# Kernel tuning notes

Measured on AMD Instinct MI355X. Metric: run time of the kernel, lower is better.

Reference implementation:

```python
import jax, jax.numpy as jnp
from jax import lax
import numpy as np

K = 1024      # kernel_size
S = 256       # stride
CUT = 513     # kernel_size//2 + 1
TC = 2 * CUT  # transform_channels = 1026
CH = 8        # combine_hidden
B = 32
TIME = 262144


def setup_inputs() -> dict:
    key = jax.random.key(0)
    ks = jax.random.split(key, 12)
    x = jax.random.normal(ks[0], (B, 1, TIME), dtype=jnp.float32)
    conv1_w = jax.random.normal(ks[1], (TC, 1, K), dtype=jnp.float32) * 0.02
    in_gamma = 1.0 + 0.1 * jax.random.normal(ks[2], (TC,), dtype=jnp.float32)
    comb1_w = jax.random.normal(ks[3], (CH, 2), dtype=jnp.float32) * 0.5
    comb1_b = jax.random.normal(ks[4], (CH,), dtype=jnp.float32) * 0.1
    comb2_w = jax.random.normal(ks[5], (1, CH), dtype=jnp.float32) * 0.5
    comb2_b = jax.random.normal(ks[6], (1,), dtype=jnp.float32) * 0.1
    lin_w = jax.random.normal(ks[7], (CUT, CUT), dtype=jnp.float32) * 0.04
    lin_b = jax.random.normal(ks[8], (CUT,), dtype=jnp.float32) * 0.02
    fc_gamma = 1.0 + 0.1 * jax.random.normal(ks[9], (CUT,), dtype=jnp.float32)
    convT_w = jax.random.normal(ks[10], (TC, 2, K), dtype=jnp.float32) * 0.02  # torch ConvTranspose1d (Cin, Cout, K)
    return {"x": x, "conv1_w": conv1_w, "in_gamma": in_gamma,
            "comb1_w": comb1_w, "comb1_b": comb1_b,
            "comb2_w": comb2_w, "comb2_b": comb2_b,
            "lin_w": lin_w, "lin_b": lin_b, "fc_gamma": fc_gamma,
            "convT_w": convT_w}


def reference(x, conv1_w, in_gamma, comb1_w, comb1_b, comb2_w, comb2_b,
              lin_w, lin_b, fc_gamma, convT_w):
    time = x.shape[2]
    # conv1: Conv1d(1, TC, K, stride=S, padding=K), no bias
    t = lax.conv_general_dilated(x, conv1_w, window_strides=(S,),
                                 padding=[(K, K)],
                                 dimension_numbers=("NCH", "OIH", "NCH"))
    # ConvScaler1d (per-channel scale) + tanh activation
    t = jnp.tanh(t * in_gamma[None, :, None])  # (B, TC, F)
    real_x, imag_x = t[:, :CUT, :], t[:, CUT:, :]
    spec = jnp.stack([real_x, imag_x], axis=1)  # (B, 2, CUT, F)
    # combine1/combine2: 1x1 Conv2d + relu
    h = jax.nn.relu(jnp.einsum("bcxf,oc->boxf", spec, comb1_w)
                    + comb1_b[None, :, None, None])
    h = jax.nn.relu(jnp.einsum("bcxf,oc->boxf", h, comb2_w)
                    + comb2_b[None, :, None, None])[:, 0]  # (B, CUT, F)
    # FC over frequency axis per (batch, frame)
    hh = h.transpose(0, 2, 1)  # (B, F, CUT)
    hh = (hh @ lin_w.T + lin_b) * fc_gamma  # BitwiseLinear + Scaler
    mask = (jnp.tanh(hh) + 1.0) * 0.5       # output_transform -> [0,1]
    mask = mask.transpose(0, 2, 1)          # (B, CUT, F)
    mask = jnp.concatenate([mask, mask], axis=1)  # (B, TC, F)
    t = t * mask
    # conv1_transpose: ConvTranspose1d(TC, 2, K, stride=S), no bias
    wt = jnp.flip(convT_w.transpose(1, 0, 2), axis=2)  # (2, TC, K) flipped
    y = lax.conv_general_dilated(t, wt, window_strides=(1,),
                                 padding=[(K - 1, K - 1)],
                                 lhs_dilation=(S,),
                                 dimension_numbers=("NCH", "OIH", "NCH"))
    y = y[:, :, K:time + K]  # (B, 2, time)
    return jax.nn.softmax(y, axis=1)
```

## Files before the change

### kernel.cpp

```cpp
#include <hip/hip_runtime.h>
#include <cstddef>
#include <cstdint>

#define TIME_N 262144
#define BATCH  32
#define KW     1024
#define ST     256
#define CUTN   513
#define TCN    1026
#define FN     1029
#define FPAD   1152
#define CPAD   1152
#define XLEN   (FPAD * ST + KW)
#define XBLK   (XLEN / 256)

#define MROWS  (BATCH * FN)
#define MP     33024
#define KPH    544
#define NPH    640
#define TBP    1040
#define FLATB  (FN * TBP)
#define KPC    4160

#define PB_XPAD  (XBLK * BATCH)
#define PB_WBF   (PB_XPAD + CPAD)
#define PB_WLIN  (PB_WBF + NPH)
#define PB_TOTAL (PB_WLIN + KPC)

typedef __bf16 bf16x8 __attribute__((ext_vector_type(8)));
typedef float floatx4 __attribute__((ext_vector_type(4)));

__device__ __forceinline__ unsigned short f2bf(float f) {
    union { float f; unsigned u; } v; v.f = f;
    unsigned r = (v.u + 0x7fffu + ((v.u >> 16) & 1u)) >> 16;
    return (unsigned short)r;
}
__device__ __forceinline__ float bf2f(unsigned short s) {
    union { unsigned u; float f; } v; v.u = ((unsigned)s) << 16;
    return v.f;
}
__device__ __forceinline__ int permch(int n) {
    return (n & 1) ? (CUTN + (n >> 1)) : (n >> 1);
}

__device__ __forceinline__ void load_lds16(const void* g, void* l) {
    __builtin_amdgcn_global_load_lds(
        (const __attribute__((address_space(1))) void*)g,
        (__attribute__((address_space(3))) void*)l, 16, 0, 0);
}

__global__ __launch_bounds__(256) void k_prep(
    const float* __restrict__ x, const float* __restrict__ c1w,
    const float* __restrict__ lw, const float* __restrict__ wct,
    unsigned short* __restrict__ xb, unsigned short* __restrict__ wbf,
    unsigned short* __restrict__ wlb, unsigned short* __restrict__ wdb)
{
    const int bid = blockIdx.x;
    if (bid < PB_XPAD) {
        const int b = bid / XBLK;
        const int p = (bid - b * XBLK) * 256 + threadIdx.x;
        const int g = p - KW;
        float v = (g >= 0 && g < TIME_N) ? x[(size_t)b * TIME_N + g] : 0.0f;
        xb[(size_t)b * XLEN + p] = f2bf(v);
    } else if (bid < PB_WBF) {
        const int n = bid - PB_XPAD;
        const int ch = (n < TCN) ? permch(n) : 0;
        for (int k = threadIdx.x; k < KW; k += 256) {
            float v = (n < TCN) ? c1w[(size_t)ch * KW + k] : 0.0f;
            wbf[(size_t)n * KW + k] = f2bf(v);
        }
    } else if (bid < PB_WLIN) {
        const int n = bid - PB_WBF;
        for (int k = threadIdx.x; k < KPH; k += 256) {
            float v = (n < CUTN && k < CUTN) ? lw[(size_t)n * CUTN + k] : 0.0f;
            wlb[(size_t)n * KPH + k] = f2bf(v);
        }
    } else {
        const int k = bid - PB_WLIN;
        const int r = threadIdx.x;
        const int j = k / TBP;
        const int n = k - j * TBP;
        float v = 0.0f;
        if (n < TCN) {
            const int ch = permch(n);
            const int widx = (3 - j) * 256 + r;
            v = wct[(size_t)(2 * ch) * KW + widx] -
                wct[(size_t)(2 * ch + 1) * KW + widx];
        }
        wdb[(size_t)r * KPC + k] = f2bf(v);
    }
}

__global__ __launch_bounds__(256) void k_conv1m(
    const unsigned short* __restrict__ xb, const unsigned short* __restrict__ wb,
    const float* __restrict__ gamma,
    const float* __restrict__ c1w, const float* __restrict__ c1b,
    const float* __restrict__ c2w, const float* __restrict__ c2b,
    unsigned short* __restrict__ tb2, unsigned short* __restrict__ h)
{
    extern __shared__ __align__(16) char lds[];

    const int b = blockIdx.x, fb = blockIdx.y, cb = blockIdx.z;
    const int f0 = fb * 128, c0 = cb * 128;
    const int tid = threadIdx.x;

    const unsigned short* xrow = xb + (size_t)b * XLEN;
    const unsigned short* ga[4];
    const unsigned short* gb[4];
    int qa[4];
#pragma unroll
    for (int i = 0; i < 4; ++i) {
        const int c = i * 256 + tid;
        const int row = c >> 3;
        const int colb = (c & 7) * 16;
        const int es = (colb ^ ((row & 7) << 4)) >> 1;
        qa[i] = c * 16;
        ga[i] = xrow + (size_t)(f0 + row) * ST + es;
        gb[i] = wb + (size_t)(c0 + row) * KW + es;
    }

    const int wave = tid >> 6, lane = tid & 63;
    const int lm = lane & 15, lq = lane >> 4;
    const int mw = (wave & 1) * 64, nw = (wave >> 1) * 64;
    const int swz = (lm & 7) << 4;
    int abo[2], bbo[2];
#pragma unroll
    for (int ks = 0; ks < 2; ++ks) {
        abo[ks] = (mw + lm) * 128 + ((ks * 64 + lq * 16) ^ swz);
        bbo[ks] = 16384 + (nw + lm) * 128 + ((ks * 64 + lq * 16) ^ swz);
    }

    floatx4 acc[4][4];
#pragma unroll
    for (int i = 0; i < 4; ++i)
#pragma unroll
        for (int j = 0; j < 4; ++j) acc[i][j] = (floatx4)0.0f;

#pragma unroll
    for (int i = 0; i < 4; ++i) {
        load_lds16(ga[i], lds + qa[i]);
        load_lds16(gb[i], lds + 16384 + qa[i]);
        ga[i] += 64; gb[i] += 64;
    }
    __syncthreads();

    for (int t = 0; t < KW / 64; ++t) {
        char* cur = lds + (t & 1) * 32768;
        char* nxt = lds + ((t + 1) & 1) * 32768;

        if (t + 1 < KW / 64) {
#pragma unroll
            for (int i = 0; i < 4; ++i) {
                load_lds16(ga[i], nxt + qa[i]);
                load_lds16(gb[i], nxt + 16384 + qa[i]);
                ga[i] += 64; gb[i] += 64;
            }
        }

        bf16x8 afr[4][2], bfr[4][2];
#pragma unroll
        for (int mt = 0; mt < 4; ++mt)
#pragma unroll
            for (int ks = 0; ks < 2; ++ks)
                afr[mt][ks] = *(const bf16x8*)(cur + abo[ks] + mt * 2048);
#pragma unroll
        for (int nt = 0; nt < 4; ++nt)
#pragma unroll
            for (int ks = 0; ks < 2; ++ks)
                bfr[nt][ks] = *(const bf16x8*)(cur + bbo[ks] + nt * 2048);
#pragma unroll
        for (int mt = 0; mt < 4; ++mt)
#pragma unroll
            for (int nt = 0; nt < 4; ++nt)
#pragma unroll
                for (int ks = 0; ks < 2; ++ks)
                    acc[mt][nt] = __builtin_amdgcn_mfma_f32_16x16x32_bf16(
                        afr[mt][ks], bfr[nt][ks], acc[mt][nt], 0, 0, 0);
        __syncthreads();
    }

    float w1[16], b1[8], w2[8];
#pragma unroll
    for (int o = 0; o < 8; ++o) {
        w1[2 * o]     = c1w[2 * o];
        w1[2 * o + 1] = c1w[2 * o + 1];
        b1[o] = c1b[o];
        w2[o] = c2w[o];
    }
    const float b2v = c2b[0];

    unsigned short* tbb = tb2 + (size_t)b * FLATB;
    const bool evenlane = ((lane & 1) == 0);
#pragma unroll
    for (int nt = 0; nt < 4; ++nt) {
        const int n = c0 + nw + nt * 16 + lm;
        const bool valid_c = (n < TCN);
        const float gv = valid_c ? gamma[permch(n)] : 0.0f;
        const int nbase = n & ~1;
        const int ybase = n >> 1;
        const bool store_c = (nbase < TBP);
#pragma unroll
        for (int mt = 0; mt < 4; ++mt) {
#pragma unroll
            for (int rp = 0; rp < 2; ++rp) {
                const int ra = rp * 2;
                const int fa = f0 + mw + mt * 16 + lq * 4 + ra;
                const float ua = acc[mt][nt][ra] * gv;
                const float ub = acc[mt][nt][ra + 1] * gv;
                const float ta  = 2.0f / (1.0f + __expf(-2.0f * ua)) - 1.0f;
                const float tbv = 2.0f / (1.0f + __expf(-2.0f * ub)) - 1.0f;
                const float sa = __shfl_xor(ta, 1);
                const float sb = __shfl_xor(tbv, 1);
                const int  fme = evenlane ? fa : (fa + 1);
                const float re = evenlane ? ta : sb;
                const float im = evenlane ? sa : tbv;
                if (fme < FN) {
                    if (store_c) {
                        const unsigned pr = (unsigned)f2bf(re) |
                                            ((unsigned)f2bf(im) << 16);
                        *(unsigned*)&tbb[(size_t)fme * TBP + nbase] = pr;
                    }
                    if (valid_c) {
                        float a2 = b2v;
#pragma unroll
                        for (int o = 0; o < 8; ++o) {
                            const float a1 = fmaxf(
                                re * w1[2 * o] + im * w1[2 * o + 1] + b1[o], 0.0f);
                            a2 += a1 * w2[o];
                        }
                        h[((size_t)b * FN + fme) * KPH + ybase] =
                            f2bf(fmaxf(a2, 0.0f));
                    }
                }
            }
        }
    }
}

__global__ __launch_bounds__(256) void k_maskm(
    const unsigned short* __restrict__ h, const unsigned short* __restrict__ wlb,
    const float* __restrict__ linb, const float* __restrict__ fcg,
    unsigned* __restrict__ tbu)
{
    __shared__ __align__(16) unsigned short As[128 * 32];
    __shared__ __align__(16) unsigned short Bs[128 * 32];

    const int m0 = blockIdx.x * 128, n0 = blockIdx.y * 128;
    const int tid = threadIdx.x;

    const int s0 = tid, s1 = tid + 256;
    const int ar0 = s0 >> 2, aq0 = s0 & 3;
    const int ar1 = s1 >> 2, aq1 = s1 & 3;
    const unsigned short* ga0 = h + (size_t)(m0 + ar0) * KPH + aq0 * 8;
    const unsigned short* ga1 = h + (size_t)(m0 + ar1) * KPH + aq1 * 8;
    const unsigned short* gb0 = wlb + (size_t)(n0 + ar0) * KPH + aq0 * 8;
    const unsigned short* gb1 = wlb + (size_t)(n0 + ar1) * KPH + aq1 * 8;
    unsigned short* la0 = &As[s0 * 8];
    unsigned short* la1 = &As[s1 * 8];
    unsigned short* lb0 = &Bs[s0 * 8];
    unsigned short* lb1 = &Bs[s1 * 8];

    const int wave = tid >> 6, lane = tid & 63;
    const int lm = lane & 15, lq = lane >> 4;
    const int mw = (wave & 1) * 64, nw = (wave >> 1) * 64;
    const unsigned short* Ap = &As[(mw + lm) * 32 + lq * 8];
    const unsigned short* Bp = &Bs[(nw + lm) * 32 + lq * 8];

    floatx4 acc[4][4];
#pragma unroll
    for (int i = 0; i < 4; ++i)
#pragma unroll
        for (int j = 0; j < 4; ++j) acc[i][j] = (floatx4)0.0f;

    for (int ks = 0; ks < KPH / 32; ++ks) {
        load_lds16(ga0, la0);
        load_lds16(ga1, la1);
        load_lds16(gb0, lb0);
        load_lds16(gb1, lb1);
        ga0 += 32; ga1 += 32; gb0 += 32; gb1 += 32;
        __syncthreads();

        bf16x8 afr[4], bfr[4];
#pragma unroll
        for (int mt = 0; mt < 4; ++mt) afr[mt] = *(const bf16x8*)(Ap + mt * 16 * 32);
#pragma unroll
        for (int nt = 0; nt < 4; ++nt) bfr[nt] = *(const bf16x8*)(Bp + nt * 16 * 32);
#pragma unroll
        for (int mt = 0; mt < 4; ++mt)
#pragma unroll
            for (int nt = 0; nt < 4; ++nt)
                acc[mt][nt] = __builtin_amdgcn_mfma_f32_16x16x32_bf16(
                    afr[mt], bfr[nt], acc[mt][nt], 0, 0, 0);
        __syncthreads();
    }

#pragma unroll
    for (int nt = 0; nt < 4; ++nt) {
        const int y = n0 + nw + nt * 16 + lm;
        if (y < CUTN) {
            const float lb = linb[y];
            const float gv = fcg[y];
#pragma unroll
            for (int mt = 0; mt < 4; ++mt) {
#pragma unroll
                for (int r = 0; r < 4; ++r) {
                    const int m = m0 + mw + mt * 16 + lq * 4 + r;
                    if (m < MROWS) {
                        const float v = (acc[mt][nt][r] + lb) * gv;
                        const float msk = 1.0f / (1.0f + __expf(-2.0f * v));
                        unsigned* p = tbu + (size_t)m * (TBP / 2) + y;
                        const unsigned u = *p;
                        const float re = bf2f((unsigned short)(u & 0xffffu)) * msk;
                        const float im = bf2f((unsigned short)(u >> 16)) * msk;
                        *p = (unsigned)f2bf(re) | ((unsigned)f2bf(im) << 16);
                    }
                }
            }
        }
    }
}

__global__ __launch_bounds__(256) void k_convtm(
    const unsigned short* __restrict__ tb2, const unsigned short* __restrict__ wdb,
    float* __restrict__ out)
{
    extern __shared__ __align__(16) char lds[];

    const int m0 = blockIdx.x * 128, n0 = blockIdx.y * 128;
    const int b   = m0 >> 10;
    const int ml0 = m0 & 1023;
    const int tid = threadIdx.x;

    const unsigned short* tbb = tb2 + (size_t)b * FLATB;
    const unsigned short* ga[4];
    const unsigned short* gb[4];
    int qa[4];
#pragma unroll
    for (int i = 0; i < 4; ++i) {
        const int c = i * 256 + tid;
        const int row = c >> 3;
        const int colb = (c & 7) * 16;
        const int es = (colb ^ ((row & 7) << 4)) >> 1;
        qa[i] = c * 16;
        ga[i] = tbb + (size_t)(ml0 + row + 1) * TBP + es;
        gb[i] = wdb + (size_t)(n0 + row) * KPC + es;
    }

    const int wave = tid >> 6, lane = tid & 63;
    const int lm = lane & 15, lq = lane >> 4;
    const int mw = (wave & 1) * 64, nw = (wave >> 1) * 64;
    const int swz = (lm & 7) << 4;
    int abo[2], bbo[2];
#pragma unroll
    for (int ks = 0; ks < 2; ++ks) {
        abo[ks] = (mw + lm) * 128 + ((ks * 64 + lq * 16) ^ swz);
        bbo[ks] = 16384 + (nw + lm) * 128 + ((ks * 64 + lq * 16) ^ swz);
    }

    floatx4 acc[4][4];
#pragma unroll
    for (int i = 0; i < 4; ++i)
#pragma unroll
        for (int j = 0; j < 4; ++j) acc[i][j] = (floatx4)0.0f;

#pragma unroll
    for (int i = 0; i < 4; ++i) {
        load_lds16(ga[i], lds + qa[i]);
        load_lds16(gb[i], lds + 16384 + qa[i]);
        ga[i] += 64; gb[i] += 64;
    }
    __syncthreads();

    for (int t = 0; t < KPC / 64; ++t) {
        char* cur = lds + (t & 1) * 32768;
        char* nxt = lds + ((t + 1) & 1) * 32768;

        if (t + 1 < KPC / 64) {
#pragma unroll
            for (int i = 0; i < 4; ++i) {
                load_lds16(ga[i], nxt + qa[i]);
                load_lds16(gb[i], nxt + 16384 + qa[i]);
                ga[i] += 64; gb[i] += 64;
            }
        }

        bf16x8 afr[4][2], bfr[4][2];
#pragma unroll
        for (int mt = 0; mt < 4; ++mt)
#pragma unroll
            for (int ks = 0; ks < 2; ++ks)
                afr[mt][ks] = *(const bf16x8*)(cur + abo[ks] + mt * 2048);
#pragma unroll
        for (int nt = 0; nt < 4; ++nt)
#pragma unroll
            for (int ks = 0; ks < 2; ++ks)
                bfr[nt][ks] = *(const bf16x8*)(cur + bbo[ks] + nt * 2048);
#pragma unroll
        for (int mt = 0; mt < 4; ++mt)
#pragma unroll
            for (int nt = 0; nt < 4; ++nt)
#pragma unroll
                for (int ks = 0; ks < 2; ++ks)
                    acc[mt][nt] = __builtin_amdgcn_mfma_f32_16x16x32_bf16(
                        afr[mt][ks], bfr[nt][ks], acc[mt][nt], 0, 0, 0);
        __syncthreads();
    }

    float* ob = out + (size_t)b * 2 * TIME_N;
#pragma unroll
    for (int nt = 0; nt < 4; ++nt) {
        const int n = n0 + nw + nt * 16 + lm;
#pragma unroll
        for (int mt = 0; mt < 4; ++mt) {
#pragma unroll
            for (int r = 0; r < 4; ++r) {
                const int m = ml0 + mw + mt * 16 + lq * 4 + r;
                const float d = acc[mt][nt][r];
                const float p0 = 1.0f / (1.0f + __expf(-d));
                const int tau = m * 256 + n;
                ob[tau]          = p0;
                ob[TIME_N + tau] = 1.0f - p0;
            }
        }
    }
}

extern "C" void kernel_launch(void* const* d_in, const int* in_sizes, int n_in,
                              void* d_out, int out_size, void* d_ws, size_t ws_size,
                              hipStream_t stream)
{
    const float* x    = (const float*)d_in[0];
    const float* c1w  = (const float*)d_in[1];
    const float* ing  = (const float*)d_in[2];
    const float* cb1w = (const float*)d_in[3];
    const float* cb1b = (const float*)d_in[4];
    const float* cb2w = (const float*)d_in[5];
    const float* cb2b = (const float*)d_in[6];
    const float* linw = (const float*)d_in[7];
    const float* linb = (const float*)d_in[8];
    const float* fcg  = (const float*)d_in[9];
    const float* ctw  = (const float*)d_in[10];
    float* out = (float*)d_out;

    unsigned short* tb2 = (unsigned short*)d_ws;
    unsigned short* h   = tb2 + (size_t)BATCH * FLATB;
    unsigned short* wlb = h + (size_t)MP * KPH;
    unsigned short* xb  = wlb + (size_t)NPH * KPH;
    unsigned short* wbf = xb + (size_t)BATCH * XLEN;
    unsigned short* wdb = wbf + (size_t)CPAD * KW;

    hipLaunchKernelGGL(k_prep, dim3(PB_TOTAL), dim3(256), 0, stream,
                       x, c1w, linw, ctw, xb, wbf, wlb, wdb);
    hipLaunchKernelGGL(k_conv1m, dim3(BATCH, 9, 9), dim3(256), 65536, stream,
                       xb, wbf, ing, cb1w, cb1b, cb2w, cb2b, tb2, h);
    hipLaunchKernelGGL(k_maskm, dim3(MP / 128, NPH / 128), dim3(256), 0, stream,
                       h, wlb, linb, fcg, (unsigned*)tb2);
    hipLaunchKernelGGL(k_convtm, dim3(256, 2), dim3(256), 65536, stream,
                       tb2, wdb, out);
}
```

Before: 446.3 us.

## Restructure GEMM main loops with explicit waitcnt barriers and XCD-aware block mapping

Both MFMA GEMM kernels (conv1 and convT) get a reworked double-buffered main loop. It issues the next tile's global-to-LDS loads, waits only for the previous tile with vmcnt(8), and uses raw s_barrier plus an lgkmcnt wait before the MFMAs, which run at raised wave priority. The last iteration is peeled so the loop carries no conditional. The conv1 grid is flattened and remapped so blocks landing on the same XCD share batch and frame rows, which should improve L2 reuse. The hand-written waitcnt counts assume a specific count of outstanding load instructions and could race if the compiler emits a different number.

```diff
diff --git a/kernel.cpp b/kernel.cpp
--- a/kernel.cpp
+++ b/kernel.cpp
@@ -100,7 +100,13 @@
 {
     extern __shared__ __align__(16) char lds[];
 
-    const int b = blockIdx.x, fb = blockIdx.y, cb = blockIdx.z;
+    const int flat = blockIdx.x;
+    const int xcd = flat & 7;
+    const int idx = flat >> 3;
+    const int cb  = idx % 9;
+    const int pr  = xcd * 36 + idx / 9;
+    const int b   = pr / 9;
+    const int fb  = pr % 9;
     const int f0 = fb * 128, c0 = cb * 128;
     const int tid = threadIdx.x;
 
@@ -142,20 +148,20 @@
         load_lds16(gb[i], lds + 16384 + qa[i]);
         ga[i] += 64; gb[i] += 64;
     }
-    __syncthreads();
-
-    for (int t = 0; t < KW / 64; ++t) {
+
+    for (int t = 0; t < KW / 64 - 1; ++t) {
         char* cur = lds + (t & 1) * 32768;
         char* nxt = lds + ((t + 1) & 1) * 32768;
 
-        if (t + 1 < KW / 64) {
-#pragma unroll
-            for (int i = 0; i < 4; ++i) {
-                load_lds16(ga[i], nxt + qa[i]);
-                load_lds16(gb[i], nxt + 16384 + qa[i]);
-                ga[i] += 64; gb[i] += 64;
-            }
-        }
+#pragma unroll
+        for (int i = 0; i < 4; ++i) {
+            load_lds16(ga[i], nxt + qa[i]);
+            load_lds16(gb[i], nxt + 16384 + qa[i]);
+            ga[i] += 64; gb[i] += 64;
+        }
+        asm volatile("s_waitcnt vmcnt(8)" ::: "memory");
+        __builtin_amdgcn_sched_barrier(0);
+        __builtin_amdgcn_s_barrier();
 
         bf16x8 afr[4][2], bfr[4][2];
 #pragma unroll
@@ -168,6 +174,11 @@
 #pragma unroll
             for (int ks = 0; ks < 2; ++ks)
                 bfr[nt][ks] = *(const bf16x8*)(cur + bbo[ks] + nt * 2048);
+        asm volatile("s_waitcnt lgkmcnt(0)" ::: "memory");
+        __builtin_amdgcn_sched_barrier(0);
+        __builtin_amdgcn_s_barrier();
+
+        __builtin_amdgcn_s_setprio(1);
 #pragma unroll
         for (int mt = 0; mt < 4; ++mt)
 #pragma unroll
@@ -176,7 +187,33 @@
                 for (int ks = 0; ks < 2; ++ks)
                     acc[mt][nt] = __builtin_amdgcn_mfma_f32_16x16x32_bf16(
                         afr[mt][ks], bfr[nt][ks], acc[mt][nt], 0, 0, 0);
-        __syncthreads();
+        __builtin_amdgcn_s_setprio(0);
+    }
+    {
+        char* cur = lds + ((KW / 64 - 1) & 1) * 32768;
+        asm volatile("s_waitcnt vmcnt(0)" ::: "memory");
+        __builtin_amdgcn_sched_barrier(0);
+        __builtin_amdgcn_s_barrier();
+
+        bf16x8 afr[4][2], bfr[4][2];
+#pragma unroll
+        for (int mt = 0; mt < 4; ++mt)
+#pragma unroll
+            for (int ks = 0; ks < 2; ++ks)
+                afr[mt][ks] = *(const bf16x8*)(cur + abo[ks] + mt * 2048);
+#pragma unroll
+        for (int nt = 0; nt < 4; ++nt)
+#pragma unroll
+            for (int ks = 0; ks < 2; ++ks)
+                bfr[nt][ks] = *(const bf16x8*)(cur + bbo[ks] + nt * 2048);
+#pragma unroll
+        for (int mt = 0; mt < 4; ++mt)
+#pragma unroll
+            for (int nt = 0; nt < 4; ++nt)
+#pragma unroll
+                for (int ks = 0; ks < 2; ++ks)
+                    acc[mt][nt] = __builtin_amdgcn_mfma_f32_16x16x32_bf16(
+                        afr[mt][ks], bfr[nt][ks], acc[mt][nt], 0, 0, 0);
     }
 
     float w1[16], b1[8], w2[8];
@@ -216,9 +253,9 @@
                 const float im = evenlane ? sa : tbv;
                 if (fme < FN) {
                     if (store_c) {
-                        const unsigned pr = (unsigned)f2bf(re) |
-                                            ((unsigned)f2bf(im) << 16);
-                        *(unsigned*)&tbb[(size_t)fme * TBP + nbase] = pr;
+                        const unsigned pr2 = (unsigned)f2bf(re) |
+                                             ((unsigned)f2bf(im) << 16);
+                        *(unsigned*)&tbb[(size_t)fme * TBP + nbase] = pr2;
                     }
                     if (valid_c) {
                         float a2 = b2v;
@@ -369,20 +406,20 @@
         load_lds16(gb[i], lds + 16384 + qa[i]);
         ga[i] += 64; gb[i] += 64;
     }
-    __syncthreads();
-
-    for (int t = 0; t < KPC / 64; ++t) {
+
+    for (int t = 0; t < KPC / 64 - 1; ++t) {
         char* cur = lds + (t & 1) * 32768;
         char* nxt = lds + ((t + 1) & 1) * 32768;
 
-        if (t + 1 < KPC / 64) {
-#pragma unroll
-            for (int i = 0; i < 4; ++i) {
-                load_lds16(ga[i], nxt + qa[i]);
-                load_lds16(gb[i], nxt + 16384 + qa[i]);
-                ga[i] += 64; gb[i] += 64;
-            }
-        }
+#pragma unroll
+        for (int i = 0; i < 4; ++i) {
+            load_lds16(ga[i], nxt + qa[i]);
+            load_lds16(gb[i], nxt + 16384 + qa[i]);
+            ga[i] += 64; gb[i] += 64;
+        }
+        asm volatile("s_waitcnt vmcnt(8)" ::: "memory");
+        __builtin_amdgcn_sched_barrier(0);
+        __builtin_amdgcn_s_barrier();
 
         bf16x8 afr[4][2], bfr[4][2];
 #pragma unroll
@@ -395,6 +432,11 @@
 #pragma unroll
             for (int ks = 0; ks < 2; ++ks)
                 bfr[nt][ks] = *(const bf16x8*)(cur + bbo[ks] + nt * 2048);
+        asm volatile("s_waitcnt lgkmcnt(0)" ::: "memory");
+        __builtin_amdgcn_sched_barrier(0);
+        __builtin_amdgcn_s_barrier();
+
+        __builtin_amdgcn_s_setprio(1);
 #pragma unroll
         for (int mt = 0; mt < 4; ++mt)
 #pragma unroll
@@ -403,7 +445,33 @@
                 for (int ks = 0; ks < 2; ++ks)
                     acc[mt][nt] = __builtin_amdgcn_mfma_f32_16x16x32_bf16(
                         afr[mt][ks], bfr[nt][ks], acc[mt][nt], 0, 0, 0);
-        __syncthreads();
+        __builtin_amdgcn_s_setprio(0);
+    }
+    {
+        char* cur = lds + ((KPC / 64 - 1) & 1) * 32768;
+        asm volatile("s_waitcnt vmcnt(0)" ::: "memory");
+        __builtin_amdgcn_sched_barrier(0);
+        __builtin_amdgcn_s_barrier();
+
+        bf16x8 afr[4][2], bfr[4][2];
+#pragma unroll
+        for (int mt = 0; mt < 4; ++mt)
+#pragma unroll
+            for (int ks = 0; ks < 2; ++ks)
+                afr[mt][ks] = *(const bf16x8*)(cur + abo[ks] + mt * 2048);
+#pragma unroll
+        for (int nt = 0; nt < 4; ++nt)
+#pragma unroll
+            for (int ks = 0; ks < 2; ++ks)
+                bfr[nt][ks] = *(const bf16x8*)(cur + bbo[ks] + nt * 2048);
+#pragma unroll
+        for (int mt = 0; mt < 4; ++mt)
+#pragma unroll
+            for (int nt = 0; nt < 4; ++nt)
+#pragma unroll
+                for (int ks = 0; ks < 2; ++ks)
+                    acc[mt][nt] = __builtin_amdgcn_mfma_f32_16x16x32_bf16(
+                        afr[mt][ks], bfr[nt][ks], acc[mt][nt], 0, 0, 0);
     }
 
     float* ob = out + (size_t)b * 2 * TIME_N;
@@ -451,7 +519,7 @@
 
     hipLaunchKernelGGL(k_prep, dim3(PB_TOTAL), dim3(256), 0, stream,
                        x, c1w, linw, ctw, xb, wbf, wlb, wdb);
-    hipLaunchKernelGGL(k_conv1m, dim3(BATCH, 9, 9), dim3(256), 65536, stream,
+    hipLaunchKernelGGL(k_conv1m, dim3(BATCH * 9 * 9), dim3(256), 65536, stream,
                        xb, wbf, ing, cb1w, cb1b, cb2w, cb2b, tb2, h);
     hipLaunchKernelGGL(k_maskm, dim3(MP / 128, NPH / 128), dim3(256), 0, stream,
                        h, wlb, linb, fcg, (unsigned*)tb2);
```

New measurement: 458.1 us. 2.6% more time.

## Restructure conv1 GEMM pipeline, XCD-aware block mapping, and LDS-staged coalesced epilogues

Applied to the files above, without the earlier changes.

The conv1 GEMM kernel now uses a smaller K step of 32 with 16 KB double buffers. It uses explicit vmcnt/lgkmcnt waits, raw barriers and setprio around the MFMA block so loads overlap compute. The grid is flattened and remapped so blocks sharing a batch/frame tile land on the same XCD, aiming at better L2 reuse. Both the conv1 and conv-transpose epilogues stage results through LDS and then write 16-byte vectorised, coalesced stores instead of scattered scalar stores. This trades extra LDS traffic and barriers for fewer global store transactions, and the halved K tile doubles the loop iterations.

```diff
diff --git a/kernel.cpp b/kernel.cpp
--- a/kernel.cpp
+++ b/kernel.cpp
@@ -29,6 +29,7 @@
 
 typedef __bf16 bf16x8 __attribute__((ext_vector_type(8)));
 typedef float floatx4 __attribute__((ext_vector_type(4)));
+typedef int   intx4   __attribute__((ext_vector_type(4)));
 
 __device__ __forceinline__ unsigned short f2bf(float f) {
     union { float f; unsigned u; } v; v.f = f;
@@ -100,20 +101,26 @@
 {
     extern __shared__ __align__(16) char lds[];
 
-    const int b = blockIdx.x, fb = blockIdx.y, cb = blockIdx.z;
+    const int flat = blockIdx.x;
+    const int xcd = flat & 7;
+    const int idx = flat >> 3;
+    const int cb  = idx % 9;
+    const int pr  = xcd * 36 + idx / 9;
+    const int b   = pr / 9;
+    const int fb  = pr % 9;
     const int f0 = fb * 128, c0 = cb * 128;
     const int tid = threadIdx.x;
 
     const unsigned short* xrow = xb + (size_t)b * XLEN;
-    const unsigned short* ga[4];
-    const unsigned short* gb[4];
-    int qa[4];
-#pragma unroll
-    for (int i = 0; i < 4; ++i) {
+    const unsigned short* ga[2];
+    const unsigned short* gb[2];
+    int qa[2];
+#pragma unroll
+    for (int i = 0; i < 2; ++i) {
         const int c = i * 256 + tid;
-        const int row = c >> 3;
-        const int colb = (c & 7) * 16;
-        const int es = (colb ^ ((row & 7) << 4)) >> 1;
+        const int row = c >> 2;
+        const int colb = (c & 3) * 16;
+        const int es = (colb ^ (((row >> 1) & 3) << 4)) >> 1;
         qa[i] = c * 16;
         ga[i] = xrow + (size_t)(f0 + row) * ST + es;
         gb[i] = wb + (size_t)(c0 + row) * KW + es;
@@ -122,13 +129,9 @@
     const int wave = tid >> 6, lane = tid & 63;
     const int lm = lane & 15, lq = lane >> 4;
     const int mw = (wave & 1) * 64, nw = (wave >> 1) * 64;
-    const int swz = (lm & 7) << 4;
-    int abo[2], bbo[2];
-#pragma unroll
-    for (int ks = 0; ks < 2; ++ks) {
-        abo[ks] = (mw + lm) * 128 + ((ks * 64 + lq * 16) ^ swz);
-        bbo[ks] = 16384 + (nw + lm) * 128 + ((ks * 64 + lq * 16) ^ swz);
-    }
+    const int swz = ((lm >> 1) & 3) << 4;
+    const int abo = (mw + lm) * 64 + ((lq * 16) ^ swz);
+    const int bbo = 8192 + (nw + lm) * 64 + ((lq * 16) ^ swz);
 
     floatx4 acc[4][4];
 #pragma unroll
@@ -137,47 +140,67 @@
         for (int j = 0; j < 4; ++j) acc[i][j] = (floatx4)0.0f;
 
 #pragma unroll
-    for (int i = 0; i < 4; ++i) {
+    for (int i = 0; i < 2; ++i) {
         load_lds16(ga[i], lds + qa[i]);
-        load_lds16(gb[i], lds + 16384 + qa[i]);
-        ga[i] += 64; gb[i] += 64;
+        load_lds16(gb[i], lds + 8192 + qa[i]);
+        ga[i] += 32; gb[i] += 32;
+    }
+
+    for (int t = 0; t < KW / 32 - 1; ++t) {
+        char* cur = lds + (t & 1) * 16384;
+        char* nxt = lds + ((t + 1) & 1) * 16384;
+
+#pragma unroll
+        for (int i = 0; i < 2; ++i) {
+            load_lds16(ga[i], nxt + qa[i]);
+            load_lds16(gb[i], nxt + 8192 + qa[i]);
+            ga[i] += 32; gb[i] += 32;
+        }
+        asm volatile("s_waitcnt vmcnt(4)" ::: "memory");
+        __builtin_amdgcn_sched_barrier(0);
+        __builtin_amdgcn_s_barrier();
+
+        bf16x8 afr[4], bfr[4];
+#pragma unroll
+        for (int mt = 0; mt < 4; ++mt)
+            afr[mt] = *(const bf16x8*)(cur + abo + mt * 1024);
+#pragma unroll
+        for (int nt = 0; nt < 4; ++nt)
+            bfr[nt] = *(const bf16x8*)(cur + bbo + nt * 1024);
+        asm volatile("s_waitcnt lgkmcnt(0)" ::: "memory");
+        __builtin_amdgcn_sched_barrier(0);
+        __builtin_amdgcn_s_barrier();
+
+        __builtin_amdgcn_s_setprio(1);
+#pragma unroll
+        for (int mt = 0; mt < 4; ++mt)
+#pragma unroll
+            for (int nt = 0; nt < 4; ++nt)
+                acc[mt][nt] = __builtin_amdgcn_mfma_f32_16x16x32_bf16(
+                    afr[mt], bfr[nt], acc[mt][nt], 0, 0, 0);
+        __builtin_amdgcn_s_setprio(0);
+    }
+    {
+        char* cur = lds + ((KW / 32 - 1) & 1) * 16384;
+        asm volatile("s_waitcnt vmcnt(0)" ::: "memory");
+        __builtin_amdgcn_sched_barrier(0);
+        __builtin_amdgcn_s_barrier();
+
+        bf16x8 afr[4], bfr[4];
+#pragma unroll
+        for (int mt = 0; mt < 4; ++mt)
+            afr[mt] = *(const bf16x8*)(cur + abo + mt * 1024);
+#pragma unroll
+        for (int nt = 0; nt < 4; ++nt)
+            bfr[nt] = *(const bf16x8*)(cur + bbo + nt * 1024);
+#pragma unroll
+        for (int mt = 0; mt < 4; ++mt)
+#pragma unroll
+            for (int nt = 0; nt < 4; ++nt)
+                acc[mt][nt] = __builtin_amdgcn_mfma_f32_16x16x32_bf16(
+                    afr[mt], bfr[nt], acc[mt][nt], 0, 0, 0);
     }
     __syncthreads();
-
-    for (int t = 0; t < KW / 64; ++t) {
-        char* cur = lds + (t & 1) * 32768;
-        char* nxt = lds + ((t + 1) & 1) * 32768;
-
-        if (t + 1 < KW / 64) {
-#pragma unroll
-            for (int i = 0; i < 4; ++i) {
-                load_lds16(ga[i], nxt + qa[i]);
-                load_lds16(gb[i], nxt + 16384 + qa[i]);
-                ga[i] += 64; gb[i] += 64;
-            }
-        }
-
-        bf16x8 afr[4][2], bfr[4][2];
-#pragma unroll
-        for (int mt = 0; mt < 4; ++mt)
-#pragma unroll
-            for (int ks = 0; ks < 2; ++ks)
-                afr[mt][ks] = *(const bf16x8*)(cur + abo[ks] + mt * 2048);
-#pragma unroll
-        for (int nt = 0; nt < 4; ++nt)
-#pragma unroll
-            for (int ks = 0; ks < 2; ++ks)
-                bfr[nt][ks] = *(const bf16x8*)(cur + bbo[ks] + nt * 2048);
-#pragma unroll
-        for (int mt = 0; mt < 4; ++mt)
-#pragma unroll
-            for (int nt = 0; nt < 4; ++nt)
-#pragma unroll
-                for (int ks = 0; ks < 2; ++ks)
-                    acc[mt][nt] = __builtin_amdgcn_mfma_f32_16x16x32_bf16(
-                        afr[mt][ks], bfr[nt][ks], acc[mt][nt], 0, 0, 0);
-        __syncthreads();
-    }
 
     float w1[16], b1[8], w2[8];
 #pragma unroll
@@ -188,51 +211,70 @@
         w2[o] = c2w[o];
     }
     const float b2v = c2b[0];
-
-    unsigned short* tbb = tb2 + (size_t)b * FLATB;
     const bool evenlane = ((lane & 1) == 0);
+
 #pragma unroll
     for (int nt = 0; nt < 4; ++nt) {
-        const int n = c0 + nw + nt * 16 + lm;
+        const int nl = nw + nt * 16 + lm;
+        const int n = c0 + nl;
         const bool valid_c = (n < TCN);
         const float gv = valid_c ? gamma[permch(n)] : 0.0f;
-        const int nbase = n & ~1;
-        const int ybase = n >> 1;
-        const bool store_c = (nbase < TBP);
+        const int nbl = nl & ~1;
+        const int yl  = nl >> 1;
 #pragma unroll
         for (int mt = 0; mt < 4; ++mt) {
 #pragma unroll
             for (int rp = 0; rp < 2; ++rp) {
                 const int ra = rp * 2;
-                const int fa = f0 + mw + mt * 16 + lq * 4 + ra;
+                const int fl = mw + mt * 16 + lq * 4 + ra;
                 const float ua = acc[mt][nt][ra] * gv;
                 const float ub = acc[mt][nt][ra + 1] * gv;
                 const float ta  = 2.0f / (1.0f + __expf(-2.0f * ua)) - 1.0f;
                 const float tbv = 2.0f / (1.0f + __expf(-2.0f * ub)) - 1.0f;
                 const float sa = __shfl_xor(ta, 1);
                 const float sb = __shfl_xor(tbv, 1);
-                const int  fme = evenlane ? fa : (fa + 1);
+                const int  fme = evenlane ? fl : (fl + 1);
                 const float re = evenlane ? ta : sb;
                 const float im = evenlane ? sa : tbv;
-                if (fme < FN) {
-                    if (store_c) {
-                        const unsigned pr = (unsigned)f2bf(re) |
-                                            ((unsigned)f2bf(im) << 16);
-                        *(unsigned*)&tbb[(size_t)fme * TBP + nbase] = pr;
-                    }
-                    if (valid_c) {
-                        float a2 = b2v;
-#pragma unroll
-                        for (int o = 0; o < 8; ++o) {
-                            const float a1 = fmaxf(
-                                re * w1[2 * o] + im * w1[2 * o + 1] + b1[o], 0.0f);
-                            a2 += a1 * w2[o];
-                        }
-                        h[((size_t)b * FN + fme) * KPH + ybase] =
-                            f2bf(fmaxf(a2, 0.0f));
-                    }
+                const unsigned pr2 = (unsigned)f2bf(re) |
+                                     ((unsigned)f2bf(im) << 16);
+                *(unsigned*)(lds + fme * 256 + nbl * 2) = pr2;
+                float a2 = b2v;
+#pragma unroll
+                for (int o = 0; o < 8; ++o) {
+                    const float a1 = fmaxf(
+                        re * w1[2 * o] + im * w1[2 * o + 1] + b1[o], 0.0f);
+                    a2 += a1 * w2[o];
                 }
+                *(unsigned short*)(lds + 32768 + fme * 128 + yl * 2) =
+                    f2bf(fmaxf(a2, 0.0f));
             }
+        }
+    }
+    __syncthreads();
+
+    const int vch = min(16, max(0, (520 - (c0 >> 1)) >> 2));
+    unsigned short* tbb = tb2 + (size_t)b * FLATB;
+#pragma unroll
+    for (int i = 0; i < 8; ++i) {
+        const int c = i * 256 + tid;
+        const int fl = c >> 4;
+        const int c16 = c & 15;
+        if (f0 + fl < FN && c16 < vch) {
+            const intx4 v = *(const intx4*)(lds + c * 16);
+            *(intx4*)(tbb + (size_t)(f0 + fl) * TBP + (c0 + c16 * 8)) = v;
+        }
+    }
+    const int vhc = min(8, max(0, (544 - (c0 >> 1)) >> 3));
+#pragma unroll
+    for (int i = 0; i < 4; ++i) {
+        const int c = i * 256 + tid;
+        const int fl = c >> 3;
+        const int c16 = c & 7;
+        if (f0 + fl < FN && c16 < vhc) {
+            const intx4 v = *(const intx4*)(lds + 32768 + c * 16);
+            *(intx4*)(h + ((size_t)b * FN + f0 + fl) * KPH +
+                      ((c0 >> 1) + c16 * 8)) = v;
         }
     }
 }
@@ -406,22 +448,35 @@
         __syncthreads();
     }
 
-    float* ob = out + (size_t)b * 2 * TIME_N;
 #pragma unroll
     for (int nt = 0; nt < 4; ++nt) {
-        const int n = n0 + nw + nt * 16 + lm;
+        const int nl = nw + nt * 16 + lm;
 #pragma unroll
         for (int mt = 0; mt < 4; ++mt) {
 #pragma unroll
             for (int r = 0; r < 4; ++r) {
-                const int m = ml0 + mw + mt * 16 + lq * 4 + r;
+                const int ml = mw + mt * 16 + lq * 4 + r;
                 const float d = acc[mt][nt][r];
                 const float p0 = 1.0f / (1.0f + __expf(-d));
-                const int tau = m * 256 + n;
-                ob[tau]          = p0;
-                ob[TIME_N + tau] = 1.0f - p0;
+                *(float*)(lds + ml * 512 + nl * 4) = p0;
             }
         }
+    }
+    __syncthreads();
+
+    float* ob = out + (size_t)b * 2 * TIME_N;
+#pragma unroll
+    for (int i = 0; i < 16; ++i) {
+        const int c = i * 256 + tid;
+        const int ml = c >> 5;
+        const int c16 = c & 31;
+        const floatx4 v = *(const floatx4*)(lds + c * 16);
+        floatx4 w;
+        w[0] = 1.0f - v[0]; w[1] = 1.0f - v[1];
+        w[2] = 1.0f - v[2]; w[3] = 1.0f - v[3];
+        const int tau = (ml0 + ml) * 256 + n0 + c16 * 4;
+        *(floatx4*)(ob + tau)          = v;
+        *(floatx4*)(ob + TIME_N + tau) = w;
     }
 }
 
@@ -451,7 +506,7 @@
 
     hipLaunchKernelGGL(k_prep, dim3(PB_TOTAL), dim3(256), 0, stream,
                        x, c1w, linw, ctw, xb, wbf, wlb, wdb);
-    hipLaunchKernelGGL(k_conv1m, dim3(BATCH, 9, 9), dim3(256), 65536, stream,
+    hipLaunchKernelGGL(k_conv1m, dim3(BATCH * 9 * 9), dim3(256), 49152, stream,
                        xb, wbf, ing, cb1w, cb1b, cb2w, cb2b, tb2, h);
     hipLaunchKernelGGL(k_maskm, dim3(MP / 128, NPH / 128), dim3(256), 0, stream,
                        h, wlb, linb, fcg, (unsigned*)tb2);
```

New measurement: 445.7 us. No clear change (-0.1%).
